# Kernel optimization log

Measured on AMD Instinct MI355X. Metric: run time of the kernel, lower is better.

Reference implementation:

```python
import jax, jax.numpy as jnp
import numpy as np

N = 64000            # total nodes (64 graphs x 1000 nodes)
E = 1048576          # edges (~16 avg degree)
NB_NODES = 1000
NUM_GRAPHS = 64
F_IN, H1, H2, H3, OUT = 128, 256, 256, 128, 64


def setup_inputs() -> dict:
    key = jax.random.key(0)
    ks = jax.random.split(key, 12)
    x = jax.random.normal(ks[0], (N, F_IN), dtype=jnp.float32)
    # random edges within each graph: pick graph per edge, then local src/dst
    g = jax.random.randint(ks[1], (E,), 0, NUM_GRAPHS)
    src = g * NB_NODES + jax.random.randint(ks[2], (E,), 0, NB_NODES)
    dst = g * NB_NODES + jax.random.randint(ks[3], (E,), 0, NB_NODES)
    edge_index = jnp.stack([src, dst]).astype(jnp.int64)
    batch = (jnp.arange(N) // NB_NODES).astype(jnp.int64)  # sorted graph ids
    def glorot(k, fan_in, fan_out):
        s = jnp.sqrt(6.0 / (fan_in + fan_out))
        return jax.random.uniform(k, (fan_in, fan_out), jnp.float32, -s, s)
    return {
        "x": x, "edge_index": edge_index, "batch": batch,
        "W1": glorot(ks[4], F_IN, H1), "b1": jnp.zeros((H1,), jnp.float32),
        "W2": glorot(ks[5], H1, H2),   "b2": jnp.zeros((H2,), jnp.float32),
        "W3": glorot(ks[6], H2, H3),   "b3": jnp.zeros((H3,), jnp.float32),
        "Wfc": glorot(ks[7], H3 * NB_NODES, OUT),
        "bfc": jnp.zeros((OUT,), jnp.float32),
    }


def _gcn_norm(edge_index, n):
    # add self-loops, symmetric normalization D^-1/2 (A+I) D^-1/2
    loop = jnp.arange(n, dtype=edge_index.dtype)
    src = jnp.concatenate([edge_index[0], loop])
    dst = jnp.concatenate([edge_index[1], loop])
    deg = jax.ops.segment_sum(jnp.ones_like(src, jnp.float32), dst, num_segments=n)
    dinv = 1.0 / jnp.sqrt(deg)  # deg >= 1 thanks to self-loops
    norm = dinv[src] * dinv[dst]
    return src, dst, norm


def _gcn_layer(h, W, b, src, dst, norm, n):
    hl = h @ W                                   # [N, H]
    msg = hl[src] * norm[:, None]                # gather + scale
    agg = jax.ops.segment_sum(msg, dst, num_segments=n)  # scatter-add
    return agg + b


def reference(x, edge_index, batch, W1, b1, W2, b2, W3, b3, Wfc, bfc):
    n = x.shape[0]
    src, dst, norm = _gcn_norm(edge_index, n)
    h = jnp.tanh(_gcn_layer(x, W1, b1, src, dst, norm, n))
    h = jnp.tanh(_gcn_layer(h, W2, b2, src, dst, norm, n))
    h = jnp.tanh(_gcn_layer(h, W3, b3, src, dst, norm, n))
    # batch is sorted with equal graph sizes -> the per-graph loop/concat
    # in the original is exactly a reshape to [num_graphs, nodes*H3]
    h_concat = h.reshape(NUM_GRAPHS, NB_NODES * H3)
    return h_concat @ Wfc + bfc
```

## Files before the change

### kernel.cpp

```cpp
#include <hip/hip_runtime.h>
#include <math.h>

#define N_NODES 64000
#define N_EDGES 1048576
#define NB 1000
#define NG 64
#define NOUT 64
#define FC_SPLIT 500
#define BK_CAP 18000

typedef __attribute__((ext_vector_type(8))) short bfrag;
typedef __attribute__((ext_vector_type(4))) float f32x4;
typedef __attribute__((ext_vector_type(2))) float f32x2;

__device__ inline float bf2f(unsigned short u) {
    union { unsigned int i; float f; } x; x.i = ((unsigned int)u) << 16; return x.f;
}
__device__ inline float bflo(unsigned int u) {
    union { unsigned int i; float f; } x; x.i = u << 16; return x.f;
}
__device__ inline float bfhi(unsigned int u) {
    union { unsigned int i; float f; } x; x.i = u & 0xffff0000u; return x.f;
}
__device__ inline f32x2 upk(unsigned int u) {
    f32x2 r; r.x = bflo(u); r.y = bfhi(u); return r;
}
__device__ inline unsigned short f2bf(float f) {
    union { float f; unsigned int i; } x; x.f = f;
    return (unsigned short)((x.i + 0x7FFFu + ((x.i >> 16) & 1u)) >> 16);
}
__device__ inline int swz(int row, int g) { return g ^ (row & 7) ^ (g >> 3); }


__global__ __launch_bounds__(256) void k_bucket(const int* __restrict__ src,
                                                const int* __restrict__ dst,
                                                int* __restrict__ gcnt,
                                                unsigned int* __restrict__ bucket) {
    __shared__ int lcnt[64];
    __shared__ int lbase[64];
    __shared__ int lcur[64];
    int t = threadIdx.x;
    int e0 = blockIdx.x * 4096;
    if (t < 64) { lcnt[t] = 0; lcur[t] = 0; }
    __syncthreads();
    for (int i = t; i < 4096; i += 256) {
        int d = dst[e0 + i];
        int g = d / NB;
        atomicAdd(&lcnt[g], 1);
    }
    __syncthreads();
    if (t < 64) lbase[t] = atomicAdd(&gcnt[t], lcnt[t]);
    __syncthreads();
    for (int i = t; i < 4096; i += 256) {
        int d = dst[e0 + i];
        int s = src[e0 + i];
        int g = d / NB;
        int pos = atomicAdd(&lcur[g], 1);
        unsigned int packed = ((unsigned int)(d - g * NB) << 10) | (unsigned int)(s - g * NB);
        bucket[(size_t)g * BK_CAP + lbase[g] + pos] = packed;
    }
}

__global__ __launch_bounds__(1024) void k_build(const int* __restrict__ gcnt,
                                                const unsigned int* __restrict__ bucket,
                                                int* __restrict__ rowptr,
                                                int* __restrict__ rowend,
                                                float* __restrict__ dinv,
                                                unsigned short* __restrict__ colp) {
    __shared__ int ind[1024];
    __shared__ int tmp[1024];
    int t = threadIdx.x;
    int g = blockIdx.x;
    int cnt = gcnt[g];
    size_t base = (size_t)g * BK_CAP;
    ind[t] = 0;
    __syncthreads();
    for (int i = t; i < cnt; i += 1024) {
        unsigned int p = bucket[base + i];
        atomicAdd(&ind[p >> 10], 1);
    }
    __syncthreads();
    int deg = ind[t];
    if (t < NB) dinv[g * NB + t] = rsqrtf((float)(deg + 1));
    tmp[t] = deg;
    __syncthreads();
    for (int off = 1; off < 1024; off <<= 1) {
        int o = (t >= off) ? tmp[t - off] : 0;
        __syncthreads();
        tmp[t] += o;
        __syncthreads();
    }
    int excl = tmp[t] - deg;
    if (t < NB) {
        rowptr[g * NB + t] = (int)base + excl;
        rowend[g * NB + t] = (int)base + excl + deg;
    }
    ind[t] = excl;
    __syncthreads();
    for (int i = t; i < cnt; i += 1024) {
        unsigned int p = bucket[base + i];
        int dl = p >> 10;
        int pos = atomicAdd(&ind[dl], 1);
        colp[base + pos] = (unsigned short)(p & 1023u);
    }
}


__global__ void k_cast_scale(const float* __restrict__ in, const float* __restrict__ dinv,
                             unsigned short* __restrict__ out) {
    int i = (blockIdx.x * blockDim.x + threadIdx.x) * 4;
    float d = dinv[i >> 7];
    float4 v = *(const float4*)(in + i);
    union { unsigned short s[4]; uint2 u; } o;
    o.s[0] = f2bf(v.x * d); o.s[1] = f2bf(v.y * d);
    o.s[2] = f2bf(v.z * d); o.s[3] = f2bf(v.w * d);
    *(uint2*)(out + i) = o.u;
}

__global__ void k_wt(const float* __restrict__ W, unsigned short* __restrict__ Wt,
                     int K, int N) {
    int i = blockIdx.x * 256 + threadIdx.x;
    if (i < K * N) {
        int n = i / K, k = i % K;
        Wt[i] = f2bf(W[k * N + n]);
    }
}


template <int H, bool TANH>
__global__ void k_agg(const unsigned short* __restrict__ hs, unsigned short* __restrict__ op,
                      const int* __restrict__ rowptr, const int* __restrict__ rowend,
                      const unsigned short* __restrict__ col,
                      const float* __restrict__ dinv, const float* __restrict__ bias) {
    constexpr int VEC = H / 64;
    int lane = threadIdx.x & 63;
    int b = blockIdx.x;
    int c = b & 7;
    int j = b >> 3;
    int g = c + 8 * (j / 250);
    int chunk = j % 250;
    int v = g * NB + chunk * 4 + (threadIdx.x >> 6);
    const unsigned short* gb = hs + (size_t)g * NB * H;
    f32x2 a0, a1;
    {
        const unsigned short* r = hs + (size_t)v * H + lane * VEC;
        if (VEC == 2) {
            a0 = upk(*(const unsigned int*)r);
        } else {
            uint2 u = *(const uint2*)r;
            a0 = upk(u.x); a1 = upk(u.y);
        }
    }
    int beg = rowptr[v], end = rowend[v];
    for (int e0 = beg; e0 < end; e0 += 64) {
        int me = e0 + lane;
        int s = (me < end) ? (int)col[me] : 0;
        int cnt = min(64, end - e0);
        int i = 0;
        for (; i + 8 <= cnt; i += 8) {
            int sx[8];
#pragma unroll
            for (int q = 0; q < 8; ++q) sx[q] = __builtin_amdgcn_readlane(s, i + q);
            if (VEC == 2) {
                unsigned int u[8];
#pragma unroll
                for (int q = 0; q < 8; ++q)
                    u[q] = *(const unsigned int*)(gb + (size_t)sx[q] * H + lane * 2);
#pragma unroll
                for (int q = 0; q < 8; ++q) a0 += upk(u[q]);
            } else {
                uint2 u[8];
#pragma unroll
                for (int q = 0; q < 8; ++q)
                    u[q] = *(const uint2*)(gb + (size_t)sx[q] * H + lane * 4);
#pragma unroll
                for (int q = 0; q < 8; ++q) { a0 += upk(u[q].x); a1 += upk(u[q].y); }
            }
        }
        for (; i + 4 <= cnt; i += 4) {
            int sx[4];
#pragma unroll
            for (int q = 0; q < 4; ++q) sx[q] = __builtin_amdgcn_readlane(s, i + q);
            if (VEC == 2) {
                unsigned int u[4];
#pragma unroll
                for (int q = 0; q < 4; ++q)
                    u[q] = *(const unsigned int*)(gb + (size_t)sx[q] * H + lane * 2);
#pragma unroll
                for (int q = 0; q < 4; ++q) a0 += upk(u[q]);
            } else {
                uint2 u[4];
#pragma unroll
                for (int q = 0; q < 4; ++q)
                    u[q] = *(const uint2*)(gb + (size_t)sx[q] * H + lane * 4);
#pragma unroll
                for (int q = 0; q < 4; ++q) { a0 += upk(u[q].x); a1 += upk(u[q].y); }
            }
        }
        for (; i < cnt; ++i) {
            int ss = __builtin_amdgcn_readlane(s, i);
            if (VEC == 2) {
                a0 += upk(*(const unsigned int*)(gb + (size_t)ss * H + lane * 2));
            } else {
                uint2 u = *(const uint2*)(gb + (size_t)ss * H + lane * 4);
                a0 += upk(u.x); a1 += upk(u.y);
            }
        }
    }
    float dv = dinv[v];
    float acc[4];
    acc[0] = a0.x; acc[1] = a0.y;
    if (VEC == 4) { acc[2] = a1.x; acc[3] = a1.y; }
    if (TANH) {
#pragma unroll
        for (int q = 0; q < VEC; ++q) acc[q] = tanhf(acc[q] * dv + bias[lane * VEC + q]);
    } else {
#pragma unroll
        for (int q = 0; q < VEC; ++q) acc[q] *= dv;
    }
    unsigned short* o = op + (size_t)v * H + lane * VEC;
    if (VEC == 2) {
        union { unsigned short s[2]; unsigned int u; } pk;
        pk.s[0] = f2bf(acc[0]); pk.s[1] = f2bf(acc[1]);
        *(unsigned int*)o = pk.u;
    } else {
        union { unsigned short s[4]; uint2 u; } pk;
        pk.s[0] = f2bf(acc[0]); pk.s[1] = f2bf(acc[1]);
        pk.s[2] = f2bf(acc[2]); pk.s[3] = f2bf(acc[3]);
        *(uint2*)o = pk.u;
    }
}


__global__ __launch_bounds__(256) void k_gemm1(const unsigned short* __restrict__ A,
                                               const unsigned short* __restrict__ W1t,
                                               const float* __restrict__ b1,
                                               const float* __restrict__ dinv,
                                               unsigned short* __restrict__ C) {
    constexpr int K = 128, N = 256;
    __shared__ unsigned short at[32 * 136];
    int t = threadIdx.x;
    int w = t >> 6, l = t & 63;
    int lm = l & 15, lq = l >> 4;
    int m0 = blockIdx.x * 32;
    int n0 = w * 64;
    {
        int row = t >> 3, kc = (t & 7) * 16;
        const unsigned short* gr = A + (size_t)(m0 + row) * K + kc;
        unsigned short* lr = at + row * 136 + kc;
        uint4 v0 = *(const uint4*)(gr);
        uint4 v1 = *(const uint4*)(gr + 8);
        *(uint4*)(lr) = v0; *(uint4*)(lr + 8) = v1;
    }
    __syncthreads();
    f32x4 acc[2][4] = {};
    const unsigned short* Bb = W1t + (size_t)(n0 + lm) * K + lq * 8;
    bfrag bfb[2][4];
#pragma unroll
    for (int j = 0; j < 4; ++j) bfb[0][j] = *(const bfrag*)(Bb + (size_t)j * 16 * K);
#pragma unroll
    for (int it = 0; it < K / 32; ++it) {
        int ks = it * 32, cur = it & 1;
        if (it + 1 < K / 32) {
#pragma unroll
            for (int j = 0; j < 4; ++j)
                bfb[cur ^ 1][j] = *(const bfrag*)(Bb + (size_t)j * 16 * K + ks + 32);
        }
        bfrag af[2];
#pragma unroll
        for (int i = 0; i < 2; ++i) af[i] = *(const bfrag*)&at[(i * 16 + lm) * 136 + ks + lq * 8];
#pragma unroll
        for (int i = 0; i < 2; ++i)
#pragma unroll
            for (int j = 0; j < 4; ++j)
                acc[i][j] = __builtin_amdgcn_mfma_f32_16x16x32_bf16(af[i], bfb[cur][j], acc[i][j], 0, 0, 0);
    }
    float bj[4];
#pragma unroll
    for (int j = 0; j < 4; ++j) bj[j] = b1[n0 + j * 16 + lm];
    int row0 = lq * 4;
    float drow[2][4];
#pragma unroll
    for (int i = 0; i < 2; ++i)
#pragma unroll
        for (int r = 0; r < 4; ++r) drow[i][r] = dinv[m0 + i * 16 + row0 + r];
#pragma unroll
    for (int i = 0; i < 2; ++i)
#pragma unroll
        for (int j = 0; j < 4; ++j)
#pragma unroll
            for (int r = 0; r < 4; ++r) {
                float v = tanhf(acc[i][j][r] + bj[j]) * drow[i][r];
                C[(size_t)(m0 + i * 16 + row0 + r) * N + n0 + j * 16 + lm] = f2bf(v);
            }
}


__global__ __launch_bounds__(256) void k_gemm23(const unsigned short* __restrict__ A,
                                                const unsigned short* __restrict__ W2t,
                                                const float* __restrict__ b2,
                                                const unsigned short* __restrict__ W3t,
                                                const float* __restrict__ dinv,
                                                unsigned short* __restrict__ C) {
    constexpr int K = 256, N3 = 128;
    __shared__ unsigned short at[32 * 256];
    int t = threadIdx.x;
    int w = t >> 6, l = t & 63;
    int lm = l & 15, lq = l >> 4;
    int m0 = blockIdx.x * 32;
    int n0 = w * 64;
    int row0 = lq * 4;
    {
        int row = t >> 3, c = t & 7;
        const unsigned short* gr = A + (size_t)(m0 + row) * K + c * 32;
        unsigned short* lr = at + row * 256;
        uint4 v[4];
#pragma unroll
        for (int j = 0; j < 4; ++j) v[j] = *(const uint4*)(gr + j * 8);
#pragma unroll
        for (int j = 0; j < 4; ++j) {
            int gidx = c * 4 + j;
            *(uint4*)(lr + swz(row, gidx) * 8) = v[j];
        }
    }
    __syncthreads();
    f32x4 acc[2][4] = {};
    {
        const unsigned short* Bb = W2t + (size_t)(n0 + lm) * K + lq * 8;
        bfrag bfb[2][4];
#pragma unroll
        for (int j = 0; j < 4; ++j) bfb[0][j] = *(const bfrag*)(Bb + (size_t)j * 16 * K);
#pragma unroll
        for (int it = 0; it < K / 32; ++it) {
            int ks = it * 32, cur = it & 1;
            if (it + 1 < K / 32) {
#pragma unroll
                for (int j = 0; j < 4; ++j)
                    bfb[cur ^ 1][j] = *(const bfrag*)(Bb + (size_t)j * 16 * K + ks + 32);
            }
            bfrag af[2];
            int gidx = it * 4 + lq;
#pragma unroll
            for (int i = 0; i < 2; ++i) {
                int row = i * 16 + lm;
                af[i] = *(const bfrag*)&at[row * 256 + swz(row, gidx) * 8];
            }
#pragma unroll
            for (int i = 0; i < 2; ++i)
#pragma unroll
                for (int j = 0; j < 4; ++j)
                    acc[i][j] = __builtin_amdgcn_mfma_f32_16x16x32_bf16(af[i], bfb[cur][j], acc[i][j], 0, 0, 0);
        }
    }
    __syncthreads();
    {
        float bj[4];
#pragma unroll
        for (int j = 0; j < 4; ++j) bj[j] = b2[n0 + j * 16 + lm];
#pragma unroll
        for (int i = 0; i < 2; ++i)
#pragma unroll
            for (int j = 0; j < 4; ++j) {
                int colb = n0 + j * 16 + lm;
                int gidx = colb >> 3, off = colb & 7;
#pragma unroll
                for (int r = 0; r < 4; ++r) {
                    int row = i * 16 + row0 + r;
                    at[row * 256 + swz(row, gidx) * 8 + off] =
                        f2bf(tanhf(acc[i][j][r] + bj[j]));
                }
            }
    }
    __syncthreads();
    {
        f32x4 acc2[2][2] = {};
        int n3 = w * 32;
        const unsigned short* Bb = W3t + (size_t)(n3 + lm) * K + lq * 8;
        bfrag bfb[2][2];
#pragma unroll
        for (int j = 0; j < 2; ++j) bfb[0][j] = *(const bfrag*)(Bb + (size_t)j * 16 * K);
#pragma unroll
        for (int it = 0; it < K / 32; ++it) {
            int ks = it * 32, cur = it & 1;
            if (it + 1 < K / 32) {
#pragma unroll
                for (int j = 0; j < 2; ++j)
                    bfb[cur ^ 1][j] = *(const bfrag*)(Bb + (size_t)j * 16 * K + ks + 32);
            }
            bfrag af[2];
            int gidx = it * 4 + lq;
#pragma unroll
            for (int i = 0; i < 2; ++i) {
                int row = i * 16 + lm;
                af[i] = *(const bfrag*)&at[row * 256 + swz(row, gidx) * 8];
            }
#pragma unroll
            for (int i = 0; i < 2; ++i)
#pragma unroll
                for (int j = 0; j < 2; ++j)
                    acc2[i][j] = __builtin_amdgcn_mfma_f32_16x16x32_bf16(af[i], bfb[cur][j], acc2[i][j], 0, 0, 0);
        }
        float drow[2][4];
#pragma unroll
        for (int i = 0; i < 2; ++i)
#pragma unroll
            for (int r = 0; r < 4; ++r) drow[i][r] = dinv[m0 + i * 16 + row0 + r];
#pragma unroll
        for (int i = 0; i < 2; ++i)
#pragma unroll
            for (int j = 0; j < 2; ++j)
#pragma unroll
                for (int r = 0; r < 4; ++r)
                    C[(size_t)(m0 + i * 16 + row0 + r) * N3 + n3 + j * 16 + lm] =
                        f2bf(acc2[i][j][r] * drow[i][r]);
    }
}


__global__ void k_fc(const unsigned short* __restrict__ A, const float* __restrict__ B,
                     float* __restrict__ part) {
    __shared__ float As[16][68];
    __shared__ float Bs[16][68];
    const int KROW = NB * 128;
    int t = threadIdx.x;
    int tx = t & 15, ty = t >> 4;
    int k0b = blockIdx.x * 256;
    float acc[4][4] = {};
    for (int k0 = k0b; k0 < k0b + 256; k0 += 16) {
        int arow = t >> 2, ak = (t & 3) << 2;
        uint2 ua = *(const uint2*)(A + (size_t)arow * KROW + k0 + ak);
        As[ak + 0][arow] = bflo(ua.x);
        As[ak + 1][arow] = bfhi(ua.x);
        As[ak + 2][arow] = bflo(ua.y);
        As[ak + 3][arow] = bfhi(ua.y);
        int bk = t >> 4, bn4 = (t & 15) << 2;
        *(float4*)&Bs[bk][bn4] = *(const float4*)(B + (size_t)(k0 + bk) * NOUT + bn4);
        __syncthreads();
#pragma unroll
        for (int kk = 0; kk < 16; ++kk) {
            float4 a = *(const float4*)&As[kk][ty << 2];
            float4 b = *(const float4*)&Bs[kk][tx << 2];
            acc[0][0] += a.x * b.x; acc[0][1] += a.x * b.y; acc[0][2] += a.x * b.z; acc[0][3] += a.x * b.w;
            acc[1][0] += a.y * b.x; acc[1][1] += a.y * b.y; acc[1][2] += a.y * b.z; acc[1][3] += a.y * b.w;
            acc[2][0] += a.z * b.x; acc[2][1] += a.z * b.y; acc[2][2] += a.z * b.z; acc[2][3] += a.z * b.w;
            acc[3][0] += a.w * b.x; acc[3][1] += a.w * b.y; acc[3][2] += a.w * b.z; acc[3][3] += a.w * b.w;
        }
        __syncthreads();
    }
    float* po = part + (size_t)blockIdx.x * (NG * NOUT);
#pragma unroll
    for (int i = 0; i < 4; ++i) {
        float4 r;
        r.x = acc[i][0]; r.y = acc[i][1]; r.z = acc[i][2]; r.w = acc[i][3];
        *(float4*)&po[((ty << 2) + i) * NOUT + (tx << 2)] = r;
    }
}

__global__ void k_fc_reduce(const float* __restrict__ part, const float* __restrict__ bfc,
                            float* __restrict__ out) {
    int i = blockIdx.x * blockDim.x + threadIdx.x;
    float s = bfc[i & 63];
    for (int b = 0; b < FC_SPLIT; ++b) s += part[(size_t)b * (NG * NOUT) + i];
    out[i] = s;
}


static inline size_t align256(size_t x) { return (x + 255) & ~(size_t)255; }

extern "C" void kernel_launch(void* const* d_in, const int* in_sizes, int n_in,
                              void* d_out, int out_size, void* d_ws, size_t ws_size,
                              hipStream_t stream) {
    const float* x   = (const float*)d_in[0];
    const int*   ei  = (const int*)d_in[1];
    const int*   src = ei;
    const int*   dst = ei + N_EDGES;
    const float* W1  = (const float*)d_in[3];
    const float* b1  = (const float*)d_in[4];
    const float* W2  = (const float*)d_in[5];
    const float* b2  = (const float*)d_in[6];
    const float* W3  = (const float*)d_in[7];
    const float* b3  = (const float*)d_in[8];
    const float* Wfc = (const float*)d_in[9];
    const float* bfc = (const float*)d_in[10];
    float* out = (float*)d_out;

    char* w = (char*)d_ws;
    unsigned short* P0 = (unsigned short*)w; w += align256((size_t)N_NODES * 256 * 2);
    unsigned short* P1 = (unsigned short*)w; w += align256((size_t)N_NODES * 256 * 2);
    unsigned short* P2 = (unsigned short*)w; w += align256((size_t)N_NODES * 256 * 2);
    int* rowptr = (int*)w;      w += align256((size_t)N_NODES * 4);
    int* rowend = (int*)w;      w += align256((size_t)N_NODES * 4);
    float* dinv = (float*)w;    w += align256((size_t)N_NODES * 4);
    int* gcnt = (int*)w;        w += align256((size_t)NG * 4);
    unsigned int* bucket = (unsigned int*)w; w += align256((size_t)NG * BK_CAP * 4);
    unsigned short* colp = (unsigned short*)w; w += align256((size_t)NG * BK_CAP * 2);
    float* fcpart = (float*)w;  w += align256((size_t)FC_SPLIT * NG * NOUT * 4);
    unsigned short* W1t = (unsigned short*)w; w += align256((size_t)128 * 256 * 2);
    unsigned short* W2t = (unsigned short*)w; w += align256((size_t)256 * 256 * 2);
    unsigned short* W3t = (unsigned short*)w; w += align256((size_t)256 * 128 * 2);

    hipMemsetAsync(gcnt, 0, (size_t)NG * 4, stream);
    k_bucket<<<N_EDGES / 4096, 256, 0, stream>>>(src, dst, gcnt, bucket);
    k_build<<<NG, 1024, 0, stream>>>(gcnt, bucket, rowptr, rowend, dinv, colp);

    k_cast_scale<<<(N_NODES * 128 / 4) / 256, 256, 0, stream>>>(x, dinv, P0);
    k_wt<<<(128 * 256 + 255) / 256, 256, 0, stream>>>(W1, W1t, 128, 256);
    k_wt<<<(256 * 256 + 255) / 256, 256, 0, stream>>>(W2, W2t, 256, 256);
    k_wt<<<(256 * 128 + 255) / 256, 256, 0, stream>>>(W3, W3t, 256, 128);

    k_agg<128, false><<<N_NODES / 4, 256, 0, stream>>>(P0, P1, rowptr, rowend, colp, dinv, nullptr);
    k_gemm1<<<N_NODES / 32, 256, 0, stream>>>(P1, W1t, b1, dinv, P2);

    k_agg<256, false><<<N_NODES / 4, 256, 0, stream>>>(P2, P0, rowptr, rowend, colp, dinv, nullptr);
    k_gemm23<<<N_NODES / 32, 256, 0, stream>>>(P0, W2t, b2, W3t, dinv, P1);

    k_agg<128, true><<<N_NODES / 4, 256, 0, stream>>>(P1, P0, rowptr, rowend, colp, dinv, b3);

    k_fc<<<FC_SPLIT, 256, 0, stream>>>(P0, Wfc, fcpart);
    k_fc_reduce<<<NG * NOUT / 256, 256, 0, stream>>>(fcpart, bfc, out);
}
```

Before: 360.6 us.

## Fuse neighbor aggregation into GEMM kernels, merge weight transposes, use fast tanh

The separate aggregation kernels for layers 1 and 2 are folded into the GEMM kernels. Each block now aggregates its 32 rows straight into swizzled LDS and then runs the MFMA GEMM on them, so the aggregated intermediate is never written to or read back from global memory. The three weight-transpose launches become a single kernel, and tanhf is replaced by an exp/rcp approximation. In exchange, the 32-row blocks lose the previous graph-interleaved block ordering used for L2 locality, each wave handles 8 serial rows, and the fast tanh may lose a little accuracy.

```diff
diff --git a/kernel.cpp b/kernel.cpp
--- a/kernel.cpp
+++ b/kernel.cpp
@@ -13,9 +13,6 @@
 typedef __attribute__((ext_vector_type(4))) float f32x4;
 typedef __attribute__((ext_vector_type(2))) float f32x2;
 
-__device__ inline float bf2f(unsigned short u) {
-    union { unsigned int i; float f; } x; x.i = ((unsigned int)u) << 16; return x.f;
-}
 __device__ inline float bflo(unsigned int u) {
     union { unsigned int i; float f; } x; x.i = u << 16; return x.f;
 }
@@ -29,7 +26,12 @@
     union { float f; unsigned int i; } x; x.f = f;
     return (unsigned short)((x.i + 0x7FFFu + ((x.i >> 16) & 1u)) >> 16);
 }
-__device__ inline int swz(int row, int g) { return g ^ (row & 7) ^ (g >> 3); }
+__device__ inline float tanh_fast(float x) {
+    float e = __expf(2.0f * x);
+    return fmaf(-2.0f, __builtin_amdgcn_rcpf(e + 1.0f), 1.0f);
+}
+__device__ inline int swz32(int row, int g) { return g ^ (row & 7) ^ (g >> 3); }
+__device__ inline int swz16(int row, int g) { return g ^ (row & 7) ^ (g >> 3); }
 
 
 __global__ __launch_bounds__(256) void k_bucket(const int* __restrict__ src,
@@ -117,21 +119,33 @@
     *(uint2*)(out + i) = o.u;
 }
 
-__global__ void k_wt(const float* __restrict__ W, unsigned short* __restrict__ Wt,
-                     int K, int N) {
+__global__ void k_wt_all(const float* __restrict__ W1, const float* __restrict__ W2,
+                         const float* __restrict__ W3, unsigned short* __restrict__ W1t,
+                         unsigned short* __restrict__ W2t, unsigned short* __restrict__ W3t) {
     int i = blockIdx.x * 256 + threadIdx.x;
-    if (i < K * N) {
-        int n = i / K, k = i % K;
-        Wt[i] = f2bf(W[k * N + n]);
+    if (i < 32768) {
+        int n = i / 128, k = i % 128;
+        W1t[i] = f2bf(W1[k * 256 + n]);
+    } else if (i < 98304) {
+        int j = i - 32768;
+        int n = j / 256, k = j % 256;
+        W2t[j] = f2bf(W2[k * 256 + n]);
+    } else {
+        int j = i - 98304;
+        int n = j / 256, k = j % 256;
+        W3t[j] = f2bf(W3[k * 128 + n]);
     }
 }
 
 
 template <int H, bool TANH>
-__global__ void k_agg(const unsigned short* __restrict__ hs, unsigned short* __restrict__ op,
-                      const int* __restrict__ rowptr, const int* __restrict__ rowend,
-                      const unsigned short* __restrict__ col,
-                      const float* __restrict__ dinv, const float* __restrict__ bias) {
+__global__ __launch_bounds__(256) void k_agg(const unsigned short* __restrict__ hs,
+                                             unsigned short* __restrict__ op,
+                                             const int* __restrict__ rowptr,
+                                             const int* __restrict__ rowend,
+                                             const unsigned short* __restrict__ col,
+                                             const float* __restrict__ dinv,
+                                             const float* __restrict__ bias) {
     constexpr int VEC = H / 64;
     int lane = threadIdx.x & 63;
     int b = blockIdx.x;
@@ -142,6 +156,7 @@
     int v = g * NB + chunk * 4 + (threadIdx.x >> 6);
     const unsigned short* gb = hs + (size_t)g * NB * H;
     f32x2 a0, a1;
+    a0 = f32x2{0.f, 0.f}; a1 = f32x2{0.f, 0.f};
     {
         const unsigned short* r = hs + (size_t)v * H + lane * VEC;
         if (VEC == 2) {
@@ -213,7 +228,7 @@
     if (VEC == 4) { acc[2] = a1.x; acc[3] = a1.y; }
     if (TANH) {
 #pragma unroll
-        for (int q = 0; q < VEC; ++q) acc[q] = tanhf(acc[q] * dv + bias[lane * VEC + q]);
+        for (int q = 0; q < VEC; ++q) acc[q] = tanh_fast(acc[q] * dv + bias[lane * VEC + q]);
     } else {
 #pragma unroll
         for (int q = 0; q < VEC; ++q) acc[q] *= dv;
@@ -232,27 +247,69 @@
 }
 
 
-__global__ __launch_bounds__(256) void k_gemm1(const unsigned short* __restrict__ A,
-                                               const unsigned short* __restrict__ W1t,
-                                               const float* __restrict__ b1,
-                                               const float* __restrict__ dinv,
-                                               unsigned short* __restrict__ C) {
+__global__ __launch_bounds__(256, 4) void k_aggemm1(const unsigned short* __restrict__ P0,
+                                                    const int* __restrict__ rowptr,
+                                                    const int* __restrict__ rowend,
+                                                    const unsigned short* __restrict__ col,
+                                                    const float* __restrict__ dinv,
+                                                    const unsigned short* __restrict__ W1t,
+                                                    const float* __restrict__ b1,
+                                                    unsigned short* __restrict__ C) {
     constexpr int K = 128, N = 256;
-    __shared__ unsigned short at[32 * 136];
+    __shared__ unsigned short at[32 * 128];
     int t = threadIdx.x;
     int w = t >> 6, l = t & 63;
     int lm = l & 15, lq = l >> 4;
+    int n0 = w * 64;
+    int row0 = lq * 4;
     int m0 = blockIdx.x * 32;
-    int n0 = w * 64;
-    {
-        int row = t >> 3, kc = (t & 7) * 16;
-        const unsigned short* gr = A + (size_t)(m0 + row) * K + kc;
-        unsigned short* lr = at + row * 136 + kc;
-        uint4 v0 = *(const uint4*)(gr);
-        uint4 v1 = *(const uint4*)(gr + 8);
-        *(uint4*)(lr) = v0; *(uint4*)(lr + 8) = v1;
-    }
-    __syncthreads();
+
+    for (int r = 0; r < 8; ++r) {
+        int row = w * 8 + r;
+        int v = m0 + row;
+        int gv = v / NB;
+        const unsigned short* gb = P0 + (size_t)gv * NB * K;
+        f32x2 a0 = upk(*(const unsigned int*)(P0 + (size_t)v * K + l * 2));
+        int beg = rowptr[v], end = rowend[v];
+        for (int e0 = beg; e0 < end; e0 += 64) {
+            int me = e0 + l;
+            int s = (me < end) ? (int)col[me] : 0;
+            int cnt = min(64, end - e0);
+            int i = 0;
+            for (; i + 8 <= cnt; i += 8) {
+                int sx[8];
+#pragma unroll
+                for (int q = 0; q < 8; ++q) sx[q] = __builtin_amdgcn_readlane(s, i + q);
+                unsigned int u[8];
+#pragma unroll
+                for (int q = 0; q < 8; ++q)
+                    u[q] = *(const unsigned int*)(gb + (size_t)sx[q] * K + l * 2);
+#pragma unroll
+                for (int q = 0; q < 8; ++q) a0 += upk(u[q]);
+            }
+            for (; i + 4 <= cnt; i += 4) {
+                int sx[4];
+#pragma unroll
+                for (int q = 0; q < 4; ++q) sx[q] = __builtin_amdgcn_readlane(s, i + q);
+                unsigned int u[4];
+#pragma unroll
+                for (int q = 0; q < 4; ++q)
+                    u[q] = *(const unsigned int*)(gb + (size_t)sx[q] * K + l * 2);
+#pragma unroll
+                for (int q = 0; q < 4; ++q) a0 += upk(u[q]);
+            }
+            for (; i < cnt; ++i) {
+                int ss = __builtin_amdgcn_readlane(s, i);
+                a0 += upk(*(const unsigned int*)(gb + (size_t)ss * K + l * 2));
+            }
+        }
+        float dv = dinv[v];
+        union { unsigned short s2[2]; unsigned int u; } pk;
+        pk.s2[0] = f2bf(a0.x * dv); pk.s2[1] = f2bf(a0.y * dv);
+        *(unsigned int*)&at[row * 128 + swz16(row, l >> 2) * 8 + (l & 3) * 2] = pk.u;
+    }
+    __syncthreads();
+
     f32x4 acc[2][4] = {};
     const unsigned short* Bb = W1t + (size_t)(n0 + lm) * K + lq * 8;
     bfrag bfb[2][4];
@@ -267,8 +324,12 @@
                 bfb[cur ^ 1][j] = *(const bfrag*)(Bb + (size_t)j * 16 * K + ks + 32);
         }
         bfrag af[2];
-#pragma unroll
-        for (int i = 0; i < 2; ++i) af[i] = *(const bfrag*)&at[(i * 16 + lm) * 136 + ks + lq * 8];
+        int gidx = it * 4 + lq;
+#pragma unroll
+        for (int i = 0; i < 2; ++i) {
+            int row = i * 16 + lm;
+            af[i] = *(const bfrag*)&at[row * 128 + swz16(row, gidx) * 8];
+        }
 #pragma unroll
         for (int i = 0; i < 2; ++i)
 #pragma unroll
@@ -278,7 +339,6 @@
     float bj[4];
 #pragma unroll
     for (int j = 0; j < 4; ++j) bj[j] = b1[n0 + j * 16 + lm];
-    int row0 = lq * 4;
     float drow[2][4];
 #pragma unroll
     for (int i = 0; i < 2; ++i)
@@ -290,40 +350,82 @@
         for (int j = 0; j < 4; ++j)
 #pragma unroll
             for (int r = 0; r < 4; ++r) {
-                float v = tanhf(acc[i][j][r] + bj[j]) * drow[i][r];
+                float v = tanh_fast(acc[i][j][r] + bj[j]) * drow[i][r];
                 C[(size_t)(m0 + i * 16 + row0 + r) * N + n0 + j * 16 + lm] = f2bf(v);
             }
 }
 
 
-__global__ __launch_bounds__(256) void k_gemm23(const unsigned short* __restrict__ A,
-                                                const unsigned short* __restrict__ W2t,
-                                                const float* __restrict__ b2,
-                                                const unsigned short* __restrict__ W3t,
-                                                const float* __restrict__ dinv,
-                                                unsigned short* __restrict__ C) {
+__global__ __launch_bounds__(256, 4) void k_aggemm23(const unsigned short* __restrict__ P2,
+                                                     const int* __restrict__ rowptr,
+                                                     const int* __restrict__ rowend,
+                                                     const unsigned short* __restrict__ col,
+                                                     const float* __restrict__ dinv,
+                                                     const unsigned short* __restrict__ W2t,
+                                                     const float* __restrict__ b2,
+                                                     const unsigned short* __restrict__ W3t,
+                                                     unsigned short* __restrict__ C) {
     constexpr int K = 256, N3 = 128;
     __shared__ unsigned short at[32 * 256];
     int t = threadIdx.x;
     int w = t >> 6, l = t & 63;
     int lm = l & 15, lq = l >> 4;
-    int m0 = blockIdx.x * 32;
     int n0 = w * 64;
     int row0 = lq * 4;
-    {
-        int row = t >> 3, c = t & 7;
-        const unsigned short* gr = A + (size_t)(m0 + row) * K + c * 32;
-        unsigned short* lr = at + row * 256;
-        uint4 v[4];
-#pragma unroll
-        for (int j = 0; j < 4; ++j) v[j] = *(const uint4*)(gr + j * 8);
-#pragma unroll
-        for (int j = 0; j < 4; ++j) {
-            int gidx = c * 4 + j;
-            *(uint4*)(lr + swz(row, gidx) * 8) = v[j];
-        }
-    }
-    __syncthreads();
+    int m0 = blockIdx.x * 32;
+
+    for (int r = 0; r < 8; ++r) {
+        int row = w * 8 + r;
+        int v = m0 + row;
+        int gv = v / NB;
+        const unsigned short* gb = P2 + (size_t)gv * NB * K;
+        f32x2 a0, a1;
+        {
+            uint2 u = *(const uint2*)(P2 + (size_t)v * K + l * 4);
+            a0 = upk(u.x); a1 = upk(u.y);
+        }
+        int beg = rowptr[v], end = rowend[v];
+        for (int e0 = beg; e0 < end; e0 += 64) {
+            int me = e0 + l;
+            int s = (me < end) ? (int)col[me] : 0;
+            int cnt = min(64, end - e0);
+            int i = 0;
+            for (; i + 8 <= cnt; i += 8) {
+                int sx[8];
+#pragma unroll
+                for (int q = 0; q < 8; ++q) sx[q] = __builtin_amdgcn_readlane(s, i + q);
+                uint2 u[8];
+#pragma unroll
+                for (int q = 0; q < 8; ++q)
+                    u[q] = *(const uint2*)(gb + (size_t)sx[q] * K + l * 4);
+#pragma unroll
+                for (int q = 0; q < 8; ++q) { a0 += upk(u[q].x); a1 += upk(u[q].y); }
+            }
+            for (; i + 4 <= cnt; i += 4) {
+                int sx[4];
+#pragma unroll
+                for (int q = 0; q < 4; ++q) sx[q] = __builtin_amdgcn_readlane(s, i + q);
+                uint2 u[4];
+#pragma unroll
+                for (int q = 0; q < 4; ++q)
+                    u[q] = *(const uint2*)(gb + (size_t)sx[q] * K + l * 4);
+#pragma unroll
+                for (int q = 0; q < 4; ++q) { a0 += upk(u[q].x); a1 += upk(u[q].y); }
+            }
+            for (; i < cnt; ++i) {
+                int ss = __builtin_amdgcn_readlane(s, i);
+                uint2 u = *(const uint2*)(gb + (size_t)ss * K + l * 4);
+                a0 += upk(u.x); a1 += upk(u.y);
+            }
+        }
+        float dv = dinv[v];
+        union { unsigned short s4[4]; uint2 u; } pk;
+        pk.s4[0] = f2bf(a0.x * dv); pk.s4[1] = f2bf(a0.y * dv);
+        pk.s4[2] = f2bf(a1.x * dv); pk.s4[3] = f2bf(a1.y * dv);
+        *(uint2*)&at[row * 256 + swz32(row, l >> 1) * 8 + (l & 1) * 4] = pk.u;
+    }
+    __syncthreads();
+
     f32x4 acc[2][4] = {};
     {
         const unsigned short* Bb = W2t + (size_t)(n0 + lm) * K + lq * 8;
@@ -343,7 +445,7 @@
 #pragma unroll
             for (int i = 0; i < 2; ++i) {
                 int row = i * 16 + lm;
-                af[i] = *(const bfrag*)&at[row * 256 + swz(row, gidx) * 8];
+                af[i] = *(const bfrag*)&at[row * 256 + swz32(row, gidx) * 8];
             }
 #pragma unroll
             for (int i = 0; i < 2; ++i)
@@ -366,8 +468,8 @@
 #pragma unroll
                 for (int r = 0; r < 4; ++r) {
                     int row = i * 16 + row0 + r;
-                    at[row * 256 + swz(row, gidx) * 8 + off] =
-                        f2bf(tanhf(acc[i][j][r] + bj[j]));
+                    at[row * 256 + swz32(row, gidx) * 8 + off] =
+                        f2bf(tanh_fast(acc[i][j][r] + bj[j]));
                 }
             }
     }
@@ -392,7 +494,7 @@
 #pragma unroll
             for (int i = 0; i < 2; ++i) {
                 int row = i * 16 + lm;
-                af[i] = *(const bfrag*)&at[row * 256 + swz(row, gidx) * 8];
+                af[i] = *(const bfrag*)&at[row * 256 + swz32(row, gidx) * 8];
             }
 #pragma unroll
             for (int i = 0; i < 2; ++i)
@@ -504,15 +606,11 @@
     k_build<<<NG, 1024, 0, stream>>>(gcnt, bucket, rowptr, rowend, dinv, colp);
 
     k_cast_scale<<<(N_NODES * 128 / 4) / 256, 256, 0, stream>>>(x, dinv, P0);
-    k_wt<<<(128 * 256 + 255) / 256, 256, 0, stream>>>(W1, W1t, 128, 256);
-    k_wt<<<(256 * 256 + 255) / 256, 256, 0, stream>>>(W2, W2t, 256, 256);
-    k_wt<<<(256 * 128 + 255) / 256, 256, 0, stream>>>(W3, W3t, 256, 128);
-
-    k_agg<128, false><<<N_NODES / 4, 256, 0, stream>>>(P0, P1, rowptr, rowend, colp, dinv, nullptr);
-    k_gemm1<<<N_NODES / 32, 256, 0, stream>>>(P1, W1t, b1, dinv, P2);
-
-    k_agg<256, false><<<N_NODES / 4, 256, 0, stream>>>(P2, P0, rowptr, rowend, colp, dinv, nullptr);
-    k_gemm23<<<N_NODES / 32, 256, 0, stream>>>(P0, W2t, b2, W3t, dinv, P1);
+    k_wt_all<<<512, 256, 0, stream>>>(W1, W2, W3, W1t, W2t, W3t);
+
+    k_aggemm1<<<N_NODES / 32, 256, 0, stream>>>(P0, rowptr, rowend, colp, dinv, W1t, b1, P2);
+
+    k_aggemm23<<<N_NODES / 32, 256, 0, stream>>>(P2, rowptr, rowend, colp, dinv, W2t, b2, W3t, P1);
 
     k_agg<128, true><<<N_NODES / 4, 256, 0, stream>>>(P1, P0, rowptr, rowend, colp, dinv, b3);
 
```

Result: slower. 388.9 us (+7.8%).
